# Optimization experiments

Measured on AMD Instinct MI355X. Metric: run time of the kernel, lower is better.

The kernel has to match this reference:

```python
import jax, jax.numpy as jnp
import numpy as np

B, IDF, CDF, SIZE, H, L = 32, 64, 256, 32, 8, 256
SS = SIZE * SIZE  # size*size = 1024


def setup_inputs() -> dict:
    key = jax.random.key(0)
    k1, k2, k3 = jax.random.split(key, 3)
    return {
        "weightedContext": jax.random.normal(k1, (B, IDF, SS), dtype=jnp.float32),
        "context": jax.random.normal(k2, (B, CDF, L), dtype=jnp.float32),
        # per-head conv1x1 weights: [H, size*size, cdf]
        "W": jax.random.normal(k3, (H, SS, CDF), dtype=jnp.float32) * 0.02,
        "ih": SIZE,
        "iw": SIZE,
    }


def reference(weightedContext, context, W, ih, iw):
    batch, idf = weightedContext.shape[0], weightedContext.shape[1]
    # conv1x1 per head == per-head GEMM over channel dim: [B,H,SS,L]
    sourceC = jnp.einsum("hoc,bcl->bhol", W, context)
    # attention scores: [B,H,idf,L]
    attn = jnp.einsum("bio,bhol->bhil", weightedContext, sourceC)
    # softmax over sourceL (nn.Softmax() on 2D view -> dim=1 == L here)
    attn = jax.nn.softmax(attn, axis=-1)
    # weightedContext_T summed over heads: bmm(sourceC, attn^T) -> [B,idf,SS]
    ctx_out = jnp.einsum("bhol,bhil->bio", sourceC, attn)
    ctx_out = ctx_out.reshape(batch, idf, ih, iw)
    # attnOut: per-head attn transposed [B,L,idf], summed over heads
    attn_out = jnp.sum(attn, axis=1).transpose(0, 2, 1)
    return ctx_out, attn_out
```

## Files before the change

### kernel.cpp

```cpp
#include <hip/hip_runtime.h>
#include <hip/hip_bf16.h>

#define BB 32
#define IDF 64
#define CDF 256
#define SSZ 1024
#define NH 8
#define LL 256
#define KHC 2048

typedef __attribute__((ext_vector_type(8))) _Float16 half8v;
typedef __attribute__((ext_vector_type(4))) float f32x4;

#define GLDS16(g, l) __builtin_amdgcn_global_load_lds(                        \
    (const __attribute__((address_space(1))) void*)(g),                       \
    (__attribute__((address_space(3))) void*)(l), 16, 0, 0)

#define WAIT_ENTER3(NFULL, NHALF)                                             \
  { if (ks < NSTEP - 2)                                                       \
      asm volatile("s_waitcnt vmcnt(" #NFULL ")" ::: "memory");               \
    else if (ks == NSTEP - 2)                                                 \
      asm volatile("s_waitcnt vmcnt(" #NHALF ")" ::: "memory");               \
    else                                                                      \
      asm volatile("s_waitcnt vmcnt(0)" ::: "memory");                        \
    __builtin_amdgcn_s_barrier();                                             \
    __builtin_amdgcn_sched_barrier(0); }
#define BAR_EXIT()                                                            \
  { __builtin_amdgcn_sched_barrier(0);                                        \
    __builtin_amdgcn_s_barrier();                                             \
    __builtin_amdgcn_sched_barrier(0); }
#define LDS_BAR()                                                             \
  { asm volatile("s_waitcnt lgkmcnt(0)" ::: "memory");                        \
    __builtin_amdgcn_s_barrier();                                             \
    __builtin_amdgcn_sched_barrier(0); }

__device__ inline unsigned short f2h(float x) {
  _Float16 h = (_Float16)x;
  return *reinterpret_cast<unsigned short*>(&h);
}
__device__ inline float h2f(unsigned short u) {
  _Float16 h = *reinterpret_cast<_Float16*>(&u);
  return (float)h;
}

__global__ __launch_bounds__(256) void k_prep(const float* __restrict__ wc,
                                              const float* __restrict__ W,
                                              const float* __restrict__ ctx,
                                              unsigned short* __restrict__ wc16,
                                              unsigned short* __restrict__ W16,
                                              unsigned short* __restrict__ ctx16,
                                              unsigned short* __restrict__ Wt16,
                                              unsigned short* __restrict__ cT16) {
  __shared__ float Tt[64][65];
  int blk0 = blockIdx.x;
  int t = threadIdx.x;
  if (blk0 < 6144) {
    int sel = blk0 >> 11;
    int idx = ((blk0 & 2047) * 256 + t) * 4;
    const float* src = (sel == 0) ? wc : (sel == 1) ? W : ctx;
    unsigned short* d = (sel == 0) ? wc16 : (sel == 1) ? W16 : ctx16;
    float4 v = *reinterpret_cast<const float4*>(&src[idx]);
    __align__(8) unsigned short h[4] = {f2h(v.x), f2h(v.y), f2h(v.z), f2h(v.w)};
    *reinterpret_cast<int2*>(&d[idx]) = *reinterpret_cast<int2*>(h);
  } else if (blk0 < 6656) {
    int blk = blk0 - 6144;
    int h = blk >> 6, ot = (blk >> 2) & 15, cq = blk & 3;
    int og = ot * 64, cg = cq * 64;
    int o_l = t >> 4, c4 = (t & 15) * 4;
#pragma unroll
    for (int p = 0; p < 4; ++p) {
      int o = o_l + 16 * p;
      float4 v = *reinterpret_cast<const float4*>(
          &W[((size_t)h * SSZ + og + o) * CDF + cg + c4]);
      Tt[c4 + 0][o] = v.x; Tt[c4 + 1][o] = v.y;
      Tt[c4 + 2][o] = v.z; Tt[c4 + 3][o] = v.w;
    }
    __syncthreads();
    int c_l = t >> 2;
#pragma unroll
    for (int p = 0; p < 4; ++p) {
      int o0 = ((t & 3) + 4 * p) * 4;
      __align__(8) unsigned short hv[4];
#pragma unroll
      for (int j = 0; j < 4; ++j) hv[j] = f2h(Tt[c_l][o0 + j]);
      size_t base = ((size_t)h * CDF + cg + c_l) * SSZ + og + o0;
      *reinterpret_cast<int2*>(&Wt16[base]) = *reinterpret_cast<int2*>(hv);
    }
  } else {
    int blk = blk0 - 6656;
    int b = blk >> 4, cq = (blk >> 2) & 3, lt = blk & 3;
    int cg = cq * 64, lg = lt * 64;
    int c_l = t >> 4, l4 = (t & 15) * 4;
#pragma unroll
    for (int p = 0; p < 4; ++p) {
      int c = c_l + 16 * p;
      float4 v = *reinterpret_cast<const float4*>(
          &ctx[((size_t)b * CDF + cg + c) * LL + lg + l4]);
      Tt[l4 + 0][c] = v.x; Tt[l4 + 1][c] = v.y;
      Tt[l4 + 2][c] = v.z; Tt[l4 + 3][c] = v.w;
    }
    __syncthreads();
    int l_l = t >> 2;
#pragma unroll
    for (int p = 0; p < 4; ++p) {
      int c0 = ((t & 3) + 4 * p) * 4;
      __align__(8) unsigned short hv[4];
#pragma unroll
      for (int j = 0; j < 4; ++j) hv[j] = f2h(Tt[l_l][c0 + j]);
      size_t base = ((size_t)b * LL + lg + l_l) * CDF + cg + c0;
      *reinterpret_cast<int2*>(&cT16[base]) = *reinterpret_cast<int2*>(hv);
    }
  }
}

#define BUFS 12288

__device__ __forceinline__ void st_p1(short* dst, const short* gA, const short* gB,
                                      int wave, int lane, int k0) {
#pragma unroll
  for (int j = 0; j < 3; ++j) {
    int inst = wave * 3 + j;
    if (inst < 4 || inst >= 20) {
      int ai = (inst < 4) ? inst : (inst - 20);
      int r  = ai * 16 + (lane >> 2);
      int gc = (lane & 3) ^ ((r >> 1) & 3);
      int toff = ((inst < 4) ? 0 : 10240) + ai * 512;
      GLDS16(gA + (size_t)r * SSZ + k0 + gc * 8, dst + toff);
    } else {
      int bi = inst - 4;
      int brow = bi * 16 + (lane >> 2);
      int gc = (lane & 3) ^ ((brow >> 1) & 3);
      GLDS16(gB + (size_t)brow * SSZ + k0 + gc * 8, dst + 2048 + bi * 512);
    }
  }
}
__device__ __forceinline__ void st_p23(short* dst, const short* gB, int ld,
                                       int wave, int lane, int k0) {
#pragma unroll
  for (int j = 0; j < 2; ++j) {
    int inst = wave * 2 + j;
    int brow = inst * 16 + (lane >> 2);
    int gc = (lane & 3) ^ ((brow >> 1) & 3);
    GLDS16(gB + (size_t)brow * ld + k0 + gc * 8, dst + inst * 512);
  }
}

__global__ __launch_bounds__(512) void k123(const unsigned short* __restrict__ wc16,
                                            const unsigned short* __restrict__ Wt16,
                                            const unsigned short* __restrict__ cT16,
                                            const unsigned short* __restrict__ ctx16,
                                            unsigned short* __restrict__ P16,
                                            unsigned short* __restrict__ N216) {
  __shared__ __align__(16) short S[3 * BUFS + 16384];
  short* P_lds = &S[3 * BUFS];

  int blk = blockIdx.x;
  int b = blk >> 3, h = blk & 7;
  int t = threadIdx.x;
  int lane = t & 63, wave = t >> 6;
  int g = wave >> 2, w4 = wave & 3;
  int ln15 = lane & 15, kh = lane >> 4;
  int rowq = (lane >> 4) * 4;

  const short* gA = (const short*)wc16 + (size_t)b * IDF * SSZ;
  const short* gB = (const short*)Wt16 + (size_t)h * CDF * SSZ;
  const short* gT = (const short*)cT16 + (size_t)b * LL * CDF;
  const short* gC = (const short*)ctx16 + (size_t)b * CDF * LL;

  int offA[2], rowM[2], rmask[2], grow[2];
#pragma unroll
  for (int r = 0; r < 2; ++r) {
    int row = g * 32 + r * 16 + ln15;
    grow[r] = row;
    offA[r] = row * 32 + ((kh ^ ((row >> 1) & 3)) * 8);
    rowM[r] = row * 256;
    rmask[r] = row & 7;
  }
  int offB1[4], offB2[4];
#pragma unroll
  for (int c = 0; c < 4; ++c) {
    int row = w4 * 64 + c * 16 + ln15;
    int swz = ((kh ^ ((row >> 1) & 3)) * 8);
    offB1[c] = 2048 + row * 32 + swz;
    offB2[c] = row * 32 + swz;
  }

  f32x4 acc[2][4] = {};

  st_p1(&S[0],        gA, gB, wave, lane, 0);
  st_p1(&S[BUFS],     gA, gB, wave, lane, 32);
  st_p1(&S[2 * BUFS], gA, gB, wave, lane, 64);
  int cur = 0;
  {
    const int NSTEP = 32;
#pragma unroll 1
    for (int ks = 0; ks < NSTEP; ++ks) {
      short* Sc = &S[cur * BUFS];
      WAIT_ENTER3(6, 3)
      half8v fa[2], fb[4];
#pragma unroll
      for (int r = 0; r < 2; ++r)
        fa[r] = *reinterpret_cast<const half8v*>(&Sc[offA[r]]);
#pragma unroll
      for (int c = 0; c < 4; ++c)
        fb[c] = *reinterpret_cast<const half8v*>(&Sc[offB1[c]]);
      __builtin_amdgcn_s_setprio(1);
#pragma unroll
      for (int r = 0; r < 2; ++r)
#pragma unroll
        for (int c = 0; c < 4; ++c)
          acc[r][c] = __builtin_amdgcn_mfma_f32_16x16x32_f16(fa[r], fb[c], acc[r][c], 0, 0, 0);
      __builtin_amdgcn_s_setprio(0);
      BAR_EXIT()
      if (ks + 3 < NSTEP)
        st_p1(Sc, gA, gB, wave, lane, (ks + 3) * 32);
      cur = (cur == 2) ? 0 : cur + 1;
    }
  }
#pragma unroll
  for (int r = 0; r < 2; ++r)
#pragma unroll
    for (int c = 0; c < 4; ++c)
#pragma unroll
      for (int reg = 0; reg < 4; ++reg) {
        int row = g * 32 + r * 16 + rowq + reg;
        int col = w4 * 64 + c * 16 + ln15;
        P_lds[row * 256 + ((((col >> 3) ^ (row & 7)) << 3) + (col & 7))] =
            (short)f2h(acc[r][c][reg]);
      }
  LDS_BAR()

#pragma unroll
  for (int r = 0; r < 2; ++r)
#pragma unroll
    for (int c = 0; c < 4; ++c) acc[r][c] = (f32x4){0.f, 0.f, 0.f, 0.f};
  st_p23(&S[0],        gT, CDF, wave, lane, 0);
  st_p23(&S[BUFS],     gT, CDF, wave, lane, 32);
  st_p23(&S[2 * BUFS], gT, CDF, wave, lane, 64);
  cur = 0;
  {
    const int NSTEP = 8;
#pragma unroll 1
    for (int ks = 0; ks < NSTEP; ++ks) {
      short* Sc = &S[cur * BUFS];
      WAIT_ENTER3(4, 2)
      half8v fa[2], fb[4];
#pragma unroll
      for (int r = 0; r < 2; ++r) {
        int ck = ((ks * 4 + kh) ^ rmask[r]) << 3;
        fa[r] = *reinterpret_cast<const half8v*>(&P_lds[rowM[r] + ck]);
      }
#pragma unroll
      for (int c = 0; c < 4; ++c)
        fb[c] = *reinterpret_cast<const half8v*>(&Sc[offB2[c]]);
      __builtin_amdgcn_s_setprio(1);
#pragma unroll
      for (int r = 0; r < 2; ++r)
#pragma unroll
        for (int c = 0; c < 4; ++c)
          acc[r][c] = __builtin_amdgcn_mfma_f32_16x16x32_f16(fa[r], fb[c], acc[r][c], 0, 0, 0);
      __builtin_amdgcn_s_setprio(0);
      BAR_EXIT()
      if (ks + 3 < NSTEP)
        st_p23(Sc, gT, CDF, wave, lane, (ks + 3) * 32);
      cur = (cur == 2) ? 0 : cur + 1;
    }
  }

  st_p23(&S[0],        gC, LL, wave, lane, 0);
  st_p23(&S[BUFS],     gC, LL, wave, lane, 32);
  st_p23(&S[2 * BUFS], gC, LL, wave, lane, 64);

  float* pm = reinterpret_cast<float*>(P_lds);
  float gmax[2][4], ginv[2][4];
#pragma unroll
  for (int r = 0; r < 2; ++r)
#pragma unroll
    for (int reg = 0; reg < 4; ++reg) {
      float m = fmaxf(fmaxf(acc[r][0][reg], acc[r][1][reg]),
                      fmaxf(acc[r][2][reg], acc[r][3][reg]));
#pragma unroll
      for (int msk = 8; msk >= 1; msk >>= 1) m = fmaxf(m, __shfl_xor(m, msk, 64));
      if (ln15 == 0) pm[(g * 32 + r * 16 + rowq + reg) * 4 + w4] = m;
    }
  LDS_BAR()
#pragma unroll
  for (int r = 0; r < 2; ++r)
#pragma unroll
    for (int reg = 0; reg < 4; ++reg) {
      int row = g * 32 + r * 16 + rowq + reg;
      float4 p0 = *reinterpret_cast<const float4*>(&pm[row * 4]);
      gmax[r][reg] = fmaxf(fmaxf(p0.x, p0.y), fmaxf(p0.z, p0.w));
    }
  LDS_BAR()
#pragma unroll
  for (int r = 0; r < 2; ++r)
#pragma unroll
    for (int reg = 0; reg < 4; ++reg) {
      float s = 0.f;
#pragma unroll
      for (int c = 0; c < 4; ++c) {
        acc[r][c][reg] = __expf(acc[r][c][reg] - gmax[r][reg]);
        s += acc[r][c][reg];
      }
#pragma unroll
      for (int msk = 8; msk >= 1; msk >>= 1) s += __shfl_xor(s, msk, 64);
      if (ln15 == 0) pm[(g * 32 + r * 16 + rowq + reg) * 4 + w4] = s;
    }
  LDS_BAR()
#pragma unroll
  for (int r = 0; r < 2; ++r)
#pragma unroll
    for (int reg = 0; reg < 4; ++reg) {
      int row = g * 32 + r * 16 + rowq + reg;
      float4 p0 = *reinterpret_cast<const float4*>(&pm[row * 4]);
      ginv[r][reg] = 1.f / (p0.x + p0.y + p0.z + p0.w);
    }
  LDS_BAR()

  size_t pbase = (size_t)blk * IDF * LL;
#pragma unroll
  for (int r = 0; r < 2; ++r)
#pragma unroll
    for (int c = 0; c < 4; ++c)
#pragma unroll
      for (int reg = 0; reg < 4; ++reg) {
        float p = acc[r][c][reg] * ginv[r][reg];
        int row = g * 32 + r * 16 + rowq + reg;
        int col = w4 * 64 + c * 16 + ln15;
        unsigned short ph = f2h(p);
        P16[pbase + (size_t)row * LL + col] = ph;
        P_lds[row * 256 + ((((col >> 3) ^ (row & 7)) << 3) + (col & 7))] = (short)ph;
      }
  LDS_BAR()

#pragma unroll
  for (int r = 0; r < 2; ++r)
#pragma unroll
    for (int c = 0; c < 4; ++c) acc[r][c] = (f32x4){0.f, 0.f, 0.f, 0.f};
  cur = 0;
  {
    const int NSTEP = 8;
#pragma unroll 1
    for (int ks = 0; ks < NSTEP; ++ks) {
      short* Sc = &S[cur * BUFS];
      WAIT_ENTER3(4, 2)
      half8v fa[2], fb[4];
#pragma unroll
      for (int r = 0; r < 2; ++r) {
        int ck = ((ks * 4 + kh) ^ rmask[r]) << 3;
        fa[r] = *reinterpret_cast<const half8v*>(&P_lds[rowM[r] + ck]);
      }
#pragma unroll
      for (int c = 0; c < 4; ++c)
        fb[c] = *reinterpret_cast<const half8v*>(&Sc[offB2[c]]);
      __builtin_amdgcn_s_setprio(1);
#pragma unroll
      for (int r = 0; r < 2; ++r)
#pragma unroll
        for (int c = 0; c < 4; ++c)
          acc[r][c] = __builtin_amdgcn_mfma_f32_16x16x32_f16(fa[r], fb[c], acc[r][c], 0, 0, 0);
      __builtin_amdgcn_s_setprio(0);
      BAR_EXIT()
      if (ks + 3 < NSTEP)
        st_p23(Sc, gC, LL, wave, lane, (ks + 3) * 32);
      cur = (cur == 2) ? 0 : cur + 1;
    }
  }

  size_t nbase = (size_t)b * IDF * KHC + h * CDF;
#pragma unroll
  for (int r = 0; r < 2; ++r)
#pragma unroll
    for (int c = 0; c < 4; ++c)
#pragma unroll
      for (int reg = 0; reg < 4; ++reg) {
        int row = g * 32 + r * 16 + rowq + reg;
        int col = w4 * 64 + c * 16 + ln15;
        N216[nbase + (size_t)row * KHC + col] = f2h(acc[r][c][reg]);
      }
}

__device__ __forceinline__ void k4_stage(short* dst,
                                         const short* gA0, const short* gA1,
                                         const short* gW,
                                         int wave, int lane, int kk0, int obase) {
  int h4 = kk0 >> 8, cb = kk0 & 255;
#pragma unroll
  for (int j = 0; j < 2; ++j) {
    int inst = wave * 2 + j;
    if (inst < 8) {
      int gi = inst >> 2;
      int rb = (inst & 3) * 16;
      int r  = rb + (lane >> 2);
      int gc = (lane & 3) ^ ((r >> 1) & 3);
      const short* src = gi ? gA1 : gA0;
      GLDS16(src + (size_t)r * KHC + kk0 + gc * 8, dst + gi * 2048 + rb * 32);
    } else {
      int bi = inst - 8;
      int brow = bi * 16 + (lane >> 2);
      int gc = (lane & 3) ^ ((brow >> 1) & 3);
      GLDS16(gW + (size_t)(h4 * SSZ + obase + brow) * CDF + cb + gc * 8,
             dst + 4096 + bi * 512);
    }
  }
}

__global__ __launch_bounds__(512) void k4_mfma(const unsigned short* __restrict__ N216,
                                               const unsigned short* __restrict__ W16,
                                               float* __restrict__ out0,
                                               float* __restrict__ out1) {
  __shared__ __align__(16) short S[3 * 8192];

  int blk = blockIdx.x;
  int g = blk >> 7;
  int r7 = blk & 127;
  int bp = r7 >> 3, ot = r7 & 7;
  int obase = ot * 128;
  int t = threadIdx.x;
  int lane = t & 63, wave = t >> 6;
  int gr = wave >> 2, w4 = wave & 3;
  int ln15 = lane & 15, kh = lane >> 4;

  int b = bp * 2 + gr;
  const short* gA0 = (const short*)N216 + (size_t)(bp * 2 + 0) * IDF * KHC;
  const short* gA1 = (const short*)N216 + (size_t)(bp * 2 + 1) * IDF * KHC;
  const short* gW  = (const short*)W16;

  int offA[4], offB[2];
#pragma unroll
  for (int r = 0; r < 4; ++r) {
    int row = r * 16 + ln15;
    offA[r] = gr * 2048 + row * 32 + ((kh ^ ((row >> 1) & 3)) * 8);
  }
#pragma unroll
  for (int c = 0; c < 2; ++c) {
    int row = w4 * 32 + c * 16 + ln15;
    offB[c] = 4096 + row * 32 + ((kh ^ ((row >> 1) & 3)) * 8);
  }

  int kbase = g * (KHC / 2);
  f32x4 acc[4][2] = {};

  k4_stage(&S[0],        gA0, gA1, gW, wave, lane, kbase, obase);
  k4_stage(&S[8192],     gA0, gA1, gW, wave, lane, kbase + 32, obase);
  k4_stage(&S[2 * 8192], gA0, gA1, gW, wave, lane, kbase + 64, obase);
  int cur = 0;

  const int NSTEP = 32;
#pragma unroll 1
  for (int ks = 0; ks < NSTEP; ++ks) {
    short* Sc = &S[cur * 8192];
    WAIT_ENTER3(4, 2)
    half8v fa[4], fb[2];
#pragma unroll
    for (int r = 0; r < 4; ++r)
      fa[r] = *reinterpret_cast<const half8v*>(&Sc[offA[r]]);
#pragma unroll
    for (int c = 0; c < 2; ++c)
      fb[c] = *reinterpret_cast<const half8v*>(&Sc[offB[c]]);
    __builtin_amdgcn_s_setprio(1);
#pragma unroll
    for (int r = 0; r < 4; ++r)
#pragma unroll
      for (int c = 0; c < 2; ++c)
        acc[r][c] = __builtin_amdgcn_mfma_f32_16x16x32_f16(fa[r], fb[c], acc[r][c], 0, 0, 0);
    __builtin_amdgcn_s_setprio(0);
    BAR_EXIT()
    if (ks + 3 < NSTEP)
      k4_stage(Sc, gA0, gA1, gW, wave, lane, kbase + (ks + 3) * 32, obase);
    cur = (cur == 2) ? 0 : cur + 1;
  }

  float* dst = (g == 0) ? out0 : out1;
  int rowq = (lane >> 4) * 4;
#pragma unroll
  for (int r = 0; r < 4; ++r)
#pragma unroll
    for (int c = 0; c < 2; ++c)
#pragma unroll
      for (int reg = 0; reg < 4; ++reg)
        dst[((size_t)b * IDF + r * 16 + rowq + reg) * SSZ +
            obase + w4 * 32 + c * 16 + ln15] = acc[r][c][reg];
}

__global__ __launch_bounds__(256) void k_epi(const unsigned short* __restrict__ P16,
                                             float* __restrict__ outa,
                                             float* __restrict__ out,
                                             const float* __restrict__ Pbuf) {
  int blk0 = blockIdx.x;
  int tid = threadIdx.x;
  if (blk0 >= 128) {
    int idx = (blk0 - 128) * 256 + tid;
    float4 a = reinterpret_cast<float4*>(out)[idx];
    float4 p = reinterpret_cast<const float4*>(Pbuf)[idx];
    a.x += p.x; a.y += p.y; a.z += p.z; a.w += p.w;
    reinterpret_cast<float4*>(out)[idx] = a;
    return;
  }
  __shared__ float T[64][65];
  int b = blk0 >> 2, lt = blk0 & 3;
  int l0 = lt * 64;
  float4 acc[4];
#pragma unroll
  for (int p = 0; p < 4; ++p) acc[p] = make_float4(0.f, 0.f, 0.f, 0.f);
  for (int h = 0; h < NH; ++h) {
    size_t src = (size_t)(b * NH + h) * IDF * LL;
#pragma unroll
    for (int p = 0; p < 4; ++p) {
      int f = tid + p * 256;
      int i = f >> 4, lc = (f & 15) * 4;
      ushort4 u = *reinterpret_cast<const ushort4*>(&P16[src + i * LL + l0 + lc]);
      acc[p].x += h2f(u.x); acc[p].y += h2f(u.y);
      acc[p].z += h2f(u.z); acc[p].w += h2f(u.w);
    }
  }
#pragma unroll
  for (int p = 0; p < 4; ++p) {
    int f = tid + p * 256;
    int i = f >> 4, lc = (f & 15) * 4;
    T[i][lc + 0] = acc[p].x; T[i][lc + 1] = acc[p].y;
    T[i][lc + 2] = acc[p].z; T[i][lc + 3] = acc[p].w;
  }
  __syncthreads();
#pragma unroll
  for (int p = 0; p < 4; ++p) {
    int f = tid + p * 256;
    int lr = f >> 4, ic = (f & 15) * 4;
    float4 v = {T[ic + 0][lr], T[ic + 1][lr], T[ic + 2][lr], T[ic + 3][lr]};
    *reinterpret_cast<float4*>(&outa[((size_t)b * LL + l0 + lr) * IDF + ic]) = v;
  }
}

extern "C" void kernel_launch(void* const* d_in, const int* in_sizes, int n_in,
                              void* d_out, int out_size, void* d_ws, size_t ws_size,
                              hipStream_t stream) {
  const float* wc  = (const float*)d_in[0];
  const float* ctx = (const float*)d_in[1];
  const float* W   = (const float*)d_in[2];
  float* out = (float*)d_out;

  const size_t NE = 2097152;
  const size_t NM = 4194304;
  unsigned short* p = (unsigned short*)d_ws;
  unsigned short *wc16 = p;   p += NE;
  unsigned short *Wt16 = p;   p += NE;
  unsigned short *W16  = p;   p += NE;
  unsigned short *ctx16 = p;  p += NE;
  unsigned short *cT16 = p;   p += NE;
  unsigned short *P16  = p;   p += NM;
  unsigned short *N216 = p;   p += NM;
  float* Pbuf = (float*)p;

  k_prep  <<<7168, 256, 0, stream>>>(wc, W, ctx, wc16, W16, ctx16, Wt16, cT16);
  k123    <<<256, 512, 0, stream>>>(wc16, Wt16, cT16, ctx16, P16, N216);
  k4_mfma <<<256, 512, 0, stream>>>(N216, W16, out, Pbuf);
  k_epi   <<<2176, 256, 0, stream>>>(P16, out + (size_t)BB * IDF * SSZ, out, Pbuf);
}
```

Baseline: 76.19 us.

## Fuse attention-sum epilogue into k4 launch and shrink k123 stage-1 buffers

The head-summed transposed attention output is moved out of the epilogue kernel and computed by 128 extra blocks appended to the k4_mfma grid, so it runs alongside the GEMM blocks. The remaining epilogue becomes a plain add kernel. Separately, k123 stage-1 no longer loads a duplicate copy of the A tile: only waves 0-3 load A. This cuts the per-stage LDS buffer from 12288 to 10240 shorts and makes the vmcnt wait counts depend on the wave. The fused blocks may compete with the GEMM blocks for CUs, and getting the per-wave wait counts wrong would risk races.

Result: no change. 75.09 us, median of 2 (-1.4%).

```diff
diff --git a/kernel.cpp b/kernel.cpp
--- a/kernel.cpp
+++ b/kernel.cpp
@@ -23,6 +23,16 @@
       asm volatile("s_waitcnt vmcnt(" #NHALF ")" ::: "memory");               \
     else                                                                      \
       asm volatile("s_waitcnt vmcnt(0)" ::: "memory");                        \
+    __builtin_amdgcn_s_barrier();                                             \
+    __builtin_amdgcn_sched_barrier(0); }
+#define WAIT_P1()                                                             \
+  { if (ks < NSTEP - 2) {                                                     \
+      if (wave < 4) asm volatile("s_waitcnt vmcnt(6)" ::: "memory");          \
+      else          asm volatile("s_waitcnt vmcnt(4)" ::: "memory");          \
+    } else if (ks == NSTEP - 2) {                                             \
+      if (wave < 4) asm volatile("s_waitcnt vmcnt(3)" ::: "memory");          \
+      else          asm volatile("s_waitcnt vmcnt(2)" ::: "memory");          \
+    } else asm volatile("s_waitcnt vmcnt(0)" ::: "memory");                   \
     __builtin_amdgcn_s_barrier();                                             \
     __builtin_amdgcn_sched_barrier(0); }
 #define BAR_EXIT()                                                            \
@@ -113,25 +123,21 @@
   }
 }
 
-#define BUFS 12288
+#define BUFS 10240
 
 __device__ __forceinline__ void st_p1(short* dst, const short* gA, const short* gB,
                                       int wave, int lane, int k0) {
-#pragma unroll
-  for (int j = 0; j < 3; ++j) {
-    int inst = wave * 3 + j;
-    if (inst < 4 || inst >= 20) {
-      int ai = (inst < 4) ? inst : (inst - 20);
-      int r  = ai * 16 + (lane >> 2);
-      int gc = (lane & 3) ^ ((r >> 1) & 3);
-      int toff = ((inst < 4) ? 0 : 10240) + ai * 512;
-      GLDS16(gA + (size_t)r * SSZ + k0 + gc * 8, dst + toff);
-    } else {
-      int bi = inst - 4;
-      int brow = bi * 16 + (lane >> 2);
-      int gc = (lane & 3) ^ ((brow >> 1) & 3);
-      GLDS16(gB + (size_t)brow * SSZ + k0 + gc * 8, dst + 2048 + bi * 512);
-    }
+  if (wave < 4) {
+    int r = wave * 16 + (lane >> 2);
+    int gc = (lane & 3) ^ ((r >> 1) & 3);
+    GLDS16(gA + (size_t)r * SSZ + k0 + gc * 8, dst + wave * 512);
+  }
+#pragma unroll
+  for (int j = 0; j < 2; ++j) {
+    int bi = wave * 2 + j;
+    int brow = bi * 16 + (lane >> 2);
+    int gc = (lane & 3) ^ ((brow >> 1) & 3);
+    GLDS16(gB + (size_t)brow * SSZ + k0 + gc * 8, dst + 2048 + bi * 512);
   }
 }
 __device__ __forceinline__ void st_p23(short* dst, const short* gB, int ld,
@@ -167,11 +173,10 @@
   const short* gT = (const short*)cT16 + (size_t)b * LL * CDF;
   const short* gC = (const short*)ctx16 + (size_t)b * CDF * LL;
 
-  int offA[2], rowM[2], rmask[2], grow[2];
+  int offA[2], rowM[2], rmask[2];
 #pragma unroll
   for (int r = 0; r < 2; ++r) {
     int row = g * 32 + r * 16 + ln15;
-    grow[r] = row;
     offA[r] = row * 32 + ((kh ^ ((row >> 1) & 3)) * 8);
     rowM[r] = row * 256;
     rmask[r] = row & 7;
@@ -196,7 +201,7 @@
 #pragma unroll 1
     for (int ks = 0; ks < NSTEP; ++ks) {
       short* Sc = &S[cur * BUFS];
-      WAIT_ENTER3(6, 3)
+      WAIT_P1()
       half8v fa[2], fb[4];
 #pragma unroll
       for (int r = 0; r < 2; ++r)
@@ -408,16 +413,57 @@
 
 __global__ __launch_bounds__(512) void k4_mfma(const unsigned short* __restrict__ N216,
                                                const unsigned short* __restrict__ W16,
+                                               const unsigned short* __restrict__ P16,
                                                float* __restrict__ out0,
-                                               float* __restrict__ out1) {
+                                               float* __restrict__ out1,
+                                               float* __restrict__ outa) {
   __shared__ __align__(16) short S[3 * 8192];
 
   int blk = blockIdx.x;
+  int t = threadIdx.x;
+
+  if (blk >= 256) {
+    int bblk = blk - 256;
+    int b = bblk >> 2, lt = bblk & 3;
+    int l0 = lt * 64;
+    float* T = reinterpret_cast<float*>(S);
+    float4 acc2[2];
+#pragma unroll
+    for (int p = 0; p < 2; ++p) acc2[p] = make_float4(0.f, 0.f, 0.f, 0.f);
+    for (int h = 0; h < NH; ++h) {
+      size_t src = (size_t)(b * NH + h) * IDF * LL;
+#pragma unroll
+      for (int p = 0; p < 2; ++p) {
+        int f = t + p * 512;
+        int i = f >> 4, lc = (f & 15) * 4;
+        ushort4 u = *reinterpret_cast<const ushort4*>(&P16[src + i * LL + l0 + lc]);
+        acc2[p].x += h2f(u.x); acc2[p].y += h2f(u.y);
+        acc2[p].z += h2f(u.z); acc2[p].w += h2f(u.w);
+      }
+    }
+#pragma unroll
+    for (int p = 0; p < 2; ++p) {
+      int f = t + p * 512;
+      int i = f >> 4, lc = (f & 15) * 4;
+      T[i * 65 + lc + 0] = acc2[p].x; T[i * 65 + lc + 1] = acc2[p].y;
+      T[i * 65 + lc + 2] = acc2[p].z; T[i * 65 + lc + 3] = acc2[p].w;
+    }
+    __syncthreads();
+#pragma unroll
+    for (int p = 0; p < 2; ++p) {
+      int f = t + p * 512;
+      int lr = f >> 4, ic = (f & 15) * 4;
+      float4 v = {T[(ic + 0) * 65 + lr], T[(ic + 1) * 65 + lr],
+                  T[(ic + 2) * 65 + lr], T[(ic + 3) * 65 + lr]};
+      *reinterpret_cast<float4*>(&outa[((size_t)b * LL + l0 + lr) * IDF + ic]) = v;
+    }
+    return;
+  }
+
   int g = blk >> 7;
   int r7 = blk & 127;
   int bp = r7 >> 3, ot = r7 & 7;
   int obase = ot * 128;
-  int t = threadIdx.x;
   int lane = t & 63, wave = t >> 6;
   int gr = wave >> 2, w4 = wave & 3;
   int ln15 = lane & 15, kh = lane >> 4;
@@ -484,52 +530,13 @@
             obase + w4 * 32 + c * 16 + ln15] = acc[r][c][reg];
 }
 
-__global__ __launch_bounds__(256) void k_epi(const unsigned short* __restrict__ P16,
-                                             float* __restrict__ outa,
-                                             float* __restrict__ out,
+__global__ __launch_bounds__(256) void k_add(float* __restrict__ out,
                                              const float* __restrict__ Pbuf) {
-  int blk0 = blockIdx.x;
-  int tid = threadIdx.x;
-  if (blk0 >= 128) {
-    int idx = (blk0 - 128) * 256 + tid;
-    float4 a = reinterpret_cast<float4*>(out)[idx];
-    float4 p = reinterpret_cast<const float4*>(Pbuf)[idx];
-    a.x += p.x; a.y += p.y; a.z += p.z; a.w += p.w;
-    reinterpret_cast<float4*>(out)[idx] = a;
-    return;
-  }
-  __shared__ float T[64][65];
-  int b = blk0 >> 2, lt = blk0 & 3;
-  int l0 = lt * 64;
-  float4 acc[4];
-#pragma unroll
-  for (int p = 0; p < 4; ++p) acc[p] = make_float4(0.f, 0.f, 0.f, 0.f);
-  for (int h = 0; h < NH; ++h) {
-    size_t src = (size_t)(b * NH + h) * IDF * LL;
-#pragma unroll
-    for (int p = 0; p < 4; ++p) {
-      int f = tid + p * 256;
-      int i = f >> 4, lc = (f & 15) * 4;
-      ushort4 u = *reinterpret_cast<const ushort4*>(&P16[src + i * LL + l0 + lc]);
-      acc[p].x += h2f(u.x); acc[p].y += h2f(u.y);
-      acc[p].z += h2f(u.z); acc[p].w += h2f(u.w);
-    }
-  }
-#pragma unroll
-  for (int p = 0; p < 4; ++p) {
-    int f = tid + p * 256;
-    int i = f >> 4, lc = (f & 15) * 4;
-    T[i][lc + 0] = acc[p].x; T[i][lc + 1] = acc[p].y;
-    T[i][lc + 2] = acc[p].z; T[i][lc + 3] = acc[p].w;
-  }
-  __syncthreads();
-#pragma unroll
-  for (int p = 0; p < 4; ++p) {
-    int f = tid + p * 256;
-    int lr = f >> 4, ic = (f & 15) * 4;
-    float4 v = {T[ic + 0][lr], T[ic + 1][lr], T[ic + 2][lr], T[ic + 3][lr]};
-    *reinterpret_cast<float4*>(&outa[((size_t)b * LL + l0 + lr) * IDF + ic]) = v;
-  }
+  int idx = blockIdx.x * 256 + threadIdx.x;
+  float4 a = reinterpret_cast<float4*>(out)[idx];
+  float4 p = reinterpret_cast<const float4*>(Pbuf)[idx];
+  a.x += p.x; a.y += p.y; a.z += p.z; a.w += p.w;
+  reinterpret_cast<float4*>(out)[idx] = a;
 }
 
 extern "C" void kernel_launch(void* const* d_in, const int* in_sizes, int n_in,
@@ -554,6 +561,7 @@
 
   k_prep  <<<7168, 256, 0, stream>>>(wc, W, ctx, wc16, W16, ctx16, Wt16, cT16);
   k123    <<<256, 512, 0, stream>>>(wc16, Wt16, cT16, ctx16, P16, N216);
-  k4_mfma <<<256, 512, 0, stream>>>(N216, W16, out, Pbuf);
-  k_epi   <<<2176, 256, 0, stream>>>(P16, out + (size_t)BB * IDF * SSZ, out, Pbuf);
-}
+  k4_mfma <<<384, 512, 0, stream>>>(N216, W16, P16, out, Pbuf,
+                                    out + (size_t)BB * IDF * SSZ);
+  k_add   <<<2048, 256, 0, stream>>>(out, Pbuf);
+}
```
